# Performance work log

Measured on AMD Instinct MI355X. Metric: run time of the kernel, lower is better.

## Reference

```python
import jax, jax.numpy as jnp
import numpy as np

K = 8          # num groups
SIZE = 250     # state/hidden size (h1 = h2 = 250)
M = 576        # flattened input size (24x24)
B = 2048       # batch
HA = 100       # attention hidden
EPS = 1e-5


def _ln(x, g, b):
    mu = jnp.mean(x, axis=-1, keepdims=True)
    v = jnp.mean(jnp.square(x - mu), axis=-1, keepdims=True)
    return (x - mu) * jax.lax.rsqrt(v + EPS) * g + b


def setup_inputs() -> dict:
    key = jax.random.key(0)
    ks = jax.random.split(key, 10)
    def w(k, shape):
        return jax.random.normal(k, shape, jnp.float32) / np.sqrt(shape[0]).astype(np.float32)
    inp = {
        "x": jax.random.normal(ks[0], (B * K, M), jnp.float32),
        "state": jax.random.normal(ks[1], (B * K, SIZE), jnp.float32),
        # encoder: Linear(SIZE,250) + ReLU + LN(250)
        "enc_W": w(ks[2], (SIZE, 250)), "enc_b": jnp.zeros((250,), jnp.float32),
        "enc_g": jnp.ones((250,), jnp.float32), "enc_bt": jnp.zeros((250,), jnp.float32),
        # core: Linear(500,250) + ReLU + LN(250)
        "core_W": w(ks[3], (500, 250)), "core_b": jnp.zeros((250,), jnp.float32),
        "core_g": jnp.ones((250,), jnp.float32), "core_bt": jnp.zeros((250,), jnp.float32),
        # context: Linear(250,250) + ReLU + LN(250)
        "ctx_W": w(ks[4], (250, 250)), "ctx_b": jnp.zeros((250,), jnp.float32),
        "ctx_g": jnp.ones((250,), jnp.float32), "ctx_bt": jnp.zeros((250,), jnp.float32),
        # attention: Linear(250,100)+Tanh+LN(100)+Linear(100,1)+Sigmoid
        "att_W1": w(ks[5], (250, HA)), "att_b1": jnp.zeros((HA,), jnp.float32),
        "att_g": jnp.ones((HA,), jnp.float32), "att_bt": jnp.zeros((HA,), jnp.float32),
        "att_W2": w(ks[6], (HA, 1)), "att_b2": jnp.zeros((1,), jnp.float32),
        # output: Linear(250 + 250 + M, SIZE)
        "out_W": w(ks[7], (250 + 250 + M, SIZE)), "out_b": jnp.zeros((SIZE,), jnp.float32),
    }
    return inp


def reference(x, state, enc_W, enc_b, enc_g, enc_bt, core_W, core_b, core_g, core_bt,
              ctx_W, ctx_b, ctx_g, ctx_bt, att_W1, att_b1, att_g, att_bt,
              att_W2, att_b2, out_W, out_b):
    bk = state.shape[0]
    b = bk // K
    h1 = 250
    # 0-1. encode state -> [B*K, h1]
    s1 = _ln(jax.nn.relu(state @ enc_W + enc_b), enc_g, enc_bt)
    s1r = s1.reshape(b, K, h1)
    # 2-3. focus / context pairs via static gather index [K, K-1]
    idx = np.array([[j for j in range(K) if j != i] for i in range(K)], np.int32)
    cs = s1r[:, idx]                                    # [b, K, K-1, h1]
    fs = jnp.broadcast_to(s1r[:, :, None, :], cs.shape)  # [b, K, K-1, h1]
    # 4. concat pairs -> [b*K*(K-1), 2*h1]
    concat = jnp.concatenate([fs, cs], axis=-1).reshape(b * K * (K - 1), 2 * h1)
    # 5. core MLP
    core_out = _ln(jax.nn.relu(concat @ core_W + core_b), core_g, core_bt)
    # context MLP
    context_out = _ln(jax.nn.relu(core_out @ ctx_W + ctx_b), ctx_g, ctx_bt)
    # attention scalar per pair
    att_h = _ln(jnp.tanh(core_out @ att_W1 + att_b1), att_g, att_bt)
    att = jax.nn.sigmoid(att_h @ att_W2 + att_b2)        # [b*K*(K-1), 1]
    # 6-7. attention-weighted sum over K-1 context effects -> [B*K, h2]
    effect_sum = jnp.sum(context_out.reshape(bk, K - 1, h1) * att.reshape(bk, K - 1, 1), axis=1)
    # 8. decode
    total = jnp.concatenate([s1, effect_sum, x], axis=1)  # [B*K, h1+h2+M]
    new_state = total @ out_W + out_b                     # [B*K, SIZE]
    return new_state
```

## Files before the change

kernel.cpp:

```cpp
#include <hip/hip_runtime.h>
#include <math.h>

#define KK 8
#define H 250
#define MDIM 576
#define NB 2048
#define HA 100
#define ROWS (NB*KK)
#define PROWS (ROWS*7)
#define PQS 512
#define KP 1088
#define CSLD 352
#define EPS 1e-5f

typedef unsigned short ushort_t;
typedef short short8 __attribute__((ext_vector_type(8)));
typedef unsigned short us8 __attribute__((ext_vector_type(8)));
typedef unsigned short us4 __attribute__((ext_vector_type(4)));
typedef unsigned short us2 __attribute__((ext_vector_type(2)));
typedef float f32x4 __attribute__((ext_vector_type(4)));

__device__ __forceinline__ void wave_reduce2(float& a, float& b) {
#pragma unroll
    for (int m = 1; m < 64; m <<= 1) {
        a += __shfl_xor(a, m, 64);
        b += __shfl_xor(b, m, 64);
    }
}

__device__ __forceinline__ void async_copy16(const void* g, void* l) {
    __builtin_amdgcn_global_load_lds(
        (const __attribute__((address_space(1))) void*)g,
        (__attribute__((address_space(3))) void*)l, 16, 0, 0);
}

__device__ __forceinline__ ushort_t f2bf(float v) {
    union { float f; unsigned int u; } c; c.f = v;
    unsigned int x = c.u;
    x += 0x7fff + ((x >> 16) & 1);
    return (ushort_t)(x >> 16);
}
__device__ __forceinline__ float bf2f(ushort_t v) {
    union { unsigned int u; float f; } c; c.u = ((unsigned int)v) << 16;
    return c.f;
}
__device__ __forceinline__ float ftanh(float x) {
    const float e = __expf(2.f * x);
    return 1.f - 2.f * __builtin_amdgcn_rcpf(e + 1.f);
}
__device__ __forceinline__ float fsigmoid(float x) {
    return __builtin_amdgcn_rcpf(1.f + __expf(-x));
}

__global__ __launch_bounds__(256) void k_prep(
    const float* __restrict__ out_W, const float* __restrict__ core_W,
    const float* __restrict__ ctx_W, const float* __restrict__ att_W1,
    const float* __restrict__ enc_W, const float* __restrict__ state,
    const float* __restrict__ x,
    ushort_t* __restrict__ Wt, ushort_t* __restrict__ Wpq,
    ushort_t* __restrict__ Wca, ushort_t* __restrict__ Wenc,
    ushort_t* __restrict__ Sb, ushort_t* __restrict__ Abuf)
{
    const int b = blockIdx.x, t = threadIdx.x;
    if (b < 256) {
        const int n = b;
        for (int k = t; k < KP; k += 256) {
            const float v = (n < H && k < 1076) ? out_W[(size_t)k * H + n] : 0.f;
            Wt[(size_t)n * KP + k] = f2bf(v);
        }
    } else if (b < 768) {
        const int n = b - 256, k = t;
        float v = 0.f;
        if (k < H) {
            if (n < H)                    v = core_W[(size_t)k * H + n];
            else if (n >= 256 && n < 506) v = core_W[(size_t)(H + k) * H + (n - 256)];
        }
        Wpq[(size_t)n * 256 + k] = f2bf(v);
    } else if (b < 1152) {
        const int n = b - 768, k = t;
        float v = 0.f;
        if (k < H) {
            if (n < H)           v = ctx_W[(size_t)k * H + n];
            else if (n < H + HA) v = att_W1[(size_t)k * HA + (n - H)];
        }
        Wca[(size_t)n * 256 + k] = f2bf(v);
    } else if (b < 1408) {
        const int n = b - 1152, k = t;
        const float v = (n < H && k < H) ? enc_W[(size_t)k * H + n] : 0.f;
        Wenc[(size_t)n * 256 + k] = f2bf(v);
    } else if (b < 2432) {
        const int r0 = (b - 1408) * 16;
        for (int idx = t; idx < 16 * 256; idx += 256) {
            const int r = r0 + (idx >> 8), k = idx & 255;
            const float v = (k < H) ? state[(size_t)r * H + k] : 0.f;
            Sb[(size_t)r * 256 + k] = f2bf(v);
        }
    } else {
        const int row = b - 2432;
        for (int c = 500 + t; c < KP; c += 256) {
            const float v = (c < 500 + MDIM) ? x[(size_t)row * MDIM + (c - 500)] : 0.f;
            Abuf[(size_t)row * KP + c] = f2bf(v);
        }
    }
}

__global__ __launch_bounds__(256) void k_gemm(
    const ushort_t* __restrict__ A, int lda,
    const ushort_t* __restrict__ B, int ldb,
    void* __restrict__ Cp, int ldc,
    const float* __restrict__ bias,
    int ksteps, int ntiles, int nlim, int bf16out)
{
    __shared__ __align__(16) ushort_t As[64 * 32];
    __shared__ __align__(16) ushort_t Bs[64 * 32];
    const int tid  = threadIdx.x;
    const int lane = tid & 63, wave = tid >> 6;
    const int wm = wave >> 1, wn = wave & 1;
    const int m0 = ((int)blockIdx.x / ntiles) * 64;
    const int n0 = ((int)blockIdx.x % ntiles) * 64;

    const int srow = tid >> 2;
    const int cs   = tid & 3;
    const int cl   = cs ^ ((srow >> 1) & 3);
    const ushort_t* gA = A + (size_t)(m0 + srow) * lda + cl * 8;
    const ushort_t* gB = B + (size_t)(n0 + srow) * ldb + cl * 8;
    ushort_t* lA = &As[tid * 8];
    ushort_t* lB = &Bs[tid * 8];

    const int q  = lane >> 4;
    const int fr = lane & 15;
    int aoff[2], boff[2];
#pragma unroll
    for (int s = 0; s < 2; ++s) {
        const int ra = wm * 32 + s * 16 + fr;
        aoff[s] = (ra * 4 + (q ^ ((ra >> 1) & 3))) * 8;
        const int rb = wn * 32 + s * 16 + fr;
        boff[s] = (rb * 4 + (q ^ ((rb >> 1) & 3))) * 8;
    }

    f32x4 acc[2][2] = {};
    for (int ks = 0; ks < ksteps; ++ks) {
        const int k0 = ks * 32;
        async_copy16(gA + k0, lA);
        async_copy16(gB + k0, lB);
        __syncthreads();
        short8 a[2], b[2];
#pragma unroll
        for (int s = 0; s < 2; ++s) {
            a[s] = *(const short8*)&As[aoff[s]];
            b[s] = *(const short8*)&Bs[boff[s]];
        }
#pragma unroll
        for (int ms = 0; ms < 2; ++ms)
#pragma unroll
            for (int ns = 0; ns < 2; ++ns)
                acc[ms][ns] = __builtin_amdgcn_mfma_f32_16x16x32_bf16(
                    a[ms], b[ns], acc[ms][ns], 0, 0, 0);
        __syncthreads();
    }

#pragma unroll
    for (int ms = 0; ms < 2; ++ms)
#pragma unroll
        for (int ns = 0; ns < 2; ++ns) {
            const int n_abs = n0 + wn * 32 + ns * 16 + fr;
            if (n_abs >= nlim) continue;
            const float bv = bias ? bias[n_abs] : 0.f;
#pragma unroll
            for (int reg = 0; reg < 4; ++reg) {
                const int m_abs = m0 + wm * 32 + ms * 16 + q * 4 + reg;
                const float v = acc[ms][ns][reg] + bv;
                if (bf16out) ((ushort_t*)Cp)[(size_t)m_abs * ldc + n_abs] = f2bf(v);
                else         ((float*)Cp)[(size_t)m_abs * ldc + n_abs] = v;
            }
        }
}

__global__ __launch_bounds__(256) void k_lnenc(const ushort_t* __restrict__ Epre,
    const float* __restrict__ eb, const float* __restrict__ eg,
    const float* __restrict__ ebt, ushort_t* __restrict__ Abuf)
{
    const int wave = threadIdx.x >> 6, lane = threadIdx.x & 63;
    const int row = blockIdx.x * 4 + wave;
    const int c0 = 4 * lane;

    const us4 v = *(const us4*)&Epre[(size_t)row * 256 + c0];
    float y[4]; float sm = 0.f, sq = 0.f;
#pragma unroll
    for (int t = 0; t < 4; ++t) {
        const int cc = c0 + t;
        float z = 0.f;
        if (cc < H) z = fmaxf(bf2f(v[t]) + eb[cc], 0.f);
        y[t] = z; sm += z; sq += z * z;
    }
    wave_reduce2(sm, sq);
    const float mu = sm * (1.f / H);
    const float rs = __builtin_amdgcn_rsqf(sq * (1.f / H) - mu * mu + EPS);
    ushort_t o[4];
#pragma unroll
    for (int t = 0; t < 4; ++t) {
        const int cc = c0 + t;
        o[t] = (cc < H) ? f2bf((y[t] - mu) * rs * eg[cc] + ebt[cc]) : (ushort_t)0;
    }
    ushort_t* dst = Abuf + (size_t)row * KP + c0;
    if (c0 + 3 < H) { *(us4*)dst = (us4){o[0], o[1], o[2], o[3]}; }
    else {
        if (c0 + 1 < H) *(us2*)dst = (us2){o[0], o[1]};
    }
}

__global__ __launch_bounds__(256) void k_core(const ushort_t* __restrict__ PQb,
    const float* __restrict__ core_b, const float* __restrict__ core_g,
    const float* __restrict__ core_bt, ushort_t* __restrict__ Co)
{
    const int wave = threadIdx.x >> 6, lane = threadIdx.x & 63;
    const int g = blockIdx.x * 4 + wave;
    const int i = g & 7;
    const int c = lane * 4;

    const us4 pu = *(const us4*)&PQb[(size_t)g * PQS + c];
    us4 qu[7];
#pragma unroll
    for (int jj = 0; jj < 7; ++jj) {
        const int j = jj + (jj >= i ? 1 : 0);
        const int qr = (g & ~7) + j;
        qu[jj] = *(const us4*)&PQb[(size_t)qr * PQS + 256 + c];
    }
    float pe[4], cb[4], cg[4], cbt[4]; bool vl[4];
#pragma unroll
    for (int t = 0; t < 4; ++t) {
        vl[t]  = (c + t) < H;
        pe[t]  = bf2f(pu[t]);
        cb[t]  = vl[t] ? core_b[c + t]  : 0.f;
        cg[t]  = vl[t] ? core_g[c + t]  : 0.f;
        cbt[t] = vl[t] ? core_bt[c + t] : 0.f;
    }
    float z[7][4], red[7][2];
#pragma unroll
    for (int jj = 0; jj < 7; ++jj) {
        float sm = 0.f, sq = 0.f;
#pragma unroll
        for (int t = 0; t < 4; ++t) {
            const float zz = vl[t] ? fmaxf(pe[t] + bf2f(qu[jj][t]) + cb[t], 0.f) : 0.f;
            z[jj][t] = zz; sm += zz; sq = fmaf(zz, zz, sq);
        }
        red[jj][0] = sm; red[jj][1] = sq;
    }
#pragma unroll
    for (int m = 1; m < 64; m <<= 1)
#pragma unroll
        for (int jj = 0; jj < 7; ++jj) {
            red[jj][0] += __shfl_xor(red[jj][0], m, 64);
            red[jj][1] += __shfl_xor(red[jj][1], m, 64);
        }
#pragma unroll
    for (int jj = 0; jj < 7; ++jj) {
        const float mu = red[jj][0] * (1.f / H);
        const float rs = __builtin_amdgcn_rsqf(red[jj][1] * (1.f / H) - mu * mu + EPS);
        us4 o;
#pragma unroll
        for (int t = 0; t < 4; ++t)
            o[t] = vl[t] ? f2bf((z[jj][t] - mu) * rs * cg[t] + cbt[t]) : (ushort_t)0;
        *(us4*)&Co[((size_t)g * 7 + jj) * 256 + c] = o;
    }
}

__global__ __launch_bounds__(512, 4) void k_cs(
    const ushort_t* __restrict__ Co,
    const ushort_t* __restrict__ Wca,
    ushort_t* __restrict__ Cs)
{
    __shared__ __align__(16) ushort_t As[64 * 32];
    __shared__ __align__(16) ushort_t Bs[384 * 32];
    const int tid = threadIdx.x, lane = tid & 63, wave = tid >> 6;
    const int wm = wave >> 2, wn = wave & 3;
    const int R0 = (int)blockIdx.x * 64;

    const int ar = tid >> 2, acb = tid & 3;
    const bool aon = tid < 256;
    const int acl = acb ^ ((ar >> 1) & 3);
    const ushort_t* gA = Co + (size_t)(R0 + ar) * 256 + acl * 8;

    const int q = lane >> 4, fr = lane & 15;

    f32x4 acc[2][6] = {};
    for (int ks = 0; ks < 8; ++ks) {
        const int k0 = ks * 32;
        if (aon) async_copy16(gA + k0, &As[tid * 8]);
#pragma unroll
        for (int it = 0; it < 3; ++it) {
            const int ci  = it * 512 + tid;
            const int rb  = ci >> 2, cb2 = ci & 3;
            const int clb = cb2 ^ ((rb >> 1) & 3);
            async_copy16(Wca + (size_t)rb * 256 + k0 + clb * 8, &Bs[ci * 8]);
        }
        __syncthreads();
        short8 a[2];
#pragma unroll
        for (int ms = 0; ms < 2; ++ms) {
            const int row = wm * 32 + ms * 16 + fr;
            a[ms] = *(const short8*)&As[(row * 4 + (q ^ ((row >> 1) & 3))) * 8];
        }
#pragma unroll
        for (int nt = 0; nt < 6; ++nt) {
            const int n = wn * 96 + nt * 16 + fr;
            const short8 b = *(const short8*)&Bs[(n * 4 + (q ^ ((n >> 1) & 3))) * 8];
#pragma unroll
            for (int ms = 0; ms < 2; ++ms)
                acc[ms][nt] = __builtin_amdgcn_mfma_f32_16x16x32_bf16(
                    a[ms], b, acc[ms][nt], 0, 0, 0);
        }
        __syncthreads();
    }

#pragma unroll
    for (int ms = 0; ms < 2; ++ms)
#pragma unroll
        for (int nt = 0; nt < 6; ++nt) {
            const int col = wn * 96 + nt * 16 + fr;
            if (col >= CSLD) continue;
#pragma unroll
            for (int reg = 0; reg < 4; ++reg) {
                const int row = R0 + wm * 32 + ms * 16 + q * 4 + reg;
                Cs[(size_t)row * CSLD + col] = f2bf(acc[ms][nt][reg]);
            }
        }
}

__global__ __launch_bounds__(256) void k_eff(const ushort_t* __restrict__ Cs,
    const float* __restrict__ ctx_b, const float* __restrict__ ctx_g, const float* __restrict__ ctx_bt,
    const float* __restrict__ att_b1, const float* __restrict__ att_g, const float* __restrict__ att_bt,
    const float* __restrict__ attW2, const float* __restrict__ att_b2,
    ushort_t* __restrict__ Abuf)
{
    const int wave = threadIdx.x >> 6, lane = threadIdx.x & 63;
    const int g = blockIdx.x * 4 + wave;
    const int c0 = 4 * lane;
    const int c1 = 256 + 2 * lane;
    const bool l48 = lane < 48;

    int ce[6]; bool eC[6], eA[6]; float b_[6], g_[6], bt_[6], w2_[6], gw[6];
#pragma unroll
    for (int e = 0; e < 6; ++e) {
        ce[e] = (e < 4) ? (c0 + e) : (c1 + (e - 4));
        const bool vld = (e < 4) || l48;
        eC[e] = vld && (ce[e] < H);
        eA[e] = vld && (ce[e] >= H) && (ce[e] < H + HA);
        if (eC[e])      { b_[e] = ctx_b[ce[e]]; g_[e] = ctx_g[ce[e]]; bt_[e] = ctx_bt[ce[e]]; w2_[e] = 0.f; }
        else if (eA[e]) { const int ca = ce[e] - H;
                          b_[e] = att_b1[ca]; g_[e] = att_g[ca]; bt_[e] = att_bt[ca]; w2_[e] = attW2[ca]; }
        else            { b_[e] = g_[e] = bt_[e] = w2_[e] = 0.f; }
        gw[e] = eA[e] ? g_[e] * w2_[e] : 0.f;
    }
    float sgw = 0.f, sbw = 0.f;
#pragma unroll
    for (int e = 0; e < 6; ++e) if (eA[e]) {
        sgw += g_[e] * w2_[e];
        sbw += bt_[e] * w2_[e];
    }
    wave_reduce2(sgw, sbw);
    const float ab2 = att_b2[0] + sbw;

    us4 v0[7]; us2 v1[7];
#pragma unroll
    for (int jj = 0; jj < 7; ++jj) {
        const size_t base = ((size_t)g * 7 + jj) * CSLD;
        v0[jj] = *(const us4*)&Cs[base + c0];
        v1[jj] = l48 ? *(const us2*)&Cs[base + c1] : (us2){0, 0};
    }

    float z[7][4], red[7][5];
#pragma unroll
    for (int jj = 0; jj < 7; ++jj) {
        float smc = 0.f, sqc = 0.f, sma = 0.f, sqa = 0.f, szgw = 0.f;
#pragma unroll
        for (int e = 0; e < 6; ++e) {
            const float raw = (e < 4) ? bf2f(v0[jj][e]) : bf2f(v1[jj][e - 4]);
            float zz = 0.f;
            if (eC[e]) {
                zz = fmaxf(raw + b_[e], 0.f);
                smc += zz; sqc = fmaf(zz, zz, sqc);
            } else if (eA[e]) {
                const float za = ftanh(raw + b_[e]);
                sma += za; sqa = fmaf(za, za, sqa);
                szgw = fmaf(za, gw[e], szgw);
            }
            if (e < 4) z[jj][e] = zz;
        }
        red[jj][0] = smc; red[jj][1] = sqc; red[jj][2] = sma;
        red[jj][3] = sqa; red[jj][4] = szgw;
    }

#pragma unroll
    for (int m = 1; m < 64; m <<= 1)
#pragma unroll
        for (int jj = 0; jj < 7; ++jj)
#pragma unroll
            for (int v = 0; v < 5; ++v)
                red[jj][v] += __shfl_xor(red[jj][v], m, 64);

    float A4[4] = {0.f, 0.f, 0.f, 0.f};
    float S0 = 0.f, S1 = 0.f;
#pragma unroll
    for (int jj = 0; jj < 7; ++jj) {
        const float muC = red[jj][0] * (1.f / H);
        const float rsC = __builtin_amdgcn_rsqf(red[jj][1] * (1.f / H) - muC * muC + EPS);
        const float muA = red[jj][2] * (1.f / HA);
        const float rsA = __builtin_amdgcn_rsqf(red[jj][3] * (1.f / HA) - muA * muA + EPS);
        const float dot = rsA * (red[jj][4] - muA * sgw) + ab2;
        const float ag  = fsigmoid(dot);
        const float cj  = ag * rsC;
        S0 += ag; S1 = fmaf(cj, muC, S1);
#pragma unroll
        for (int e = 0; e < 4; ++e) A4[e] = fmaf(cj, z[jj][e], A4[e]);
    }
    ushort_t o[4];
#pragma unroll
    for (int e = 0; e < 4; ++e)
        o[e] = f2bf(g_[e] * (A4[e] - S1) + bt_[e] * S0);
    ushort_t* dst = Abuf + (size_t)g * KP + H + c0;
    if (c0 + 1 < H) *(us2*)dst       = (us2){o[0], o[1]};
    if (c0 + 3 < H) *(us2*)(dst + 2) = (us2){o[2], o[3]};
}

extern "C" void kernel_launch(void* const* d_in, const int* in_sizes, int n_in,
                              void* d_out, int out_size, void* d_ws, size_t ws_size,
                              hipStream_t stream)
{
    const float* x      = (const float*)d_in[0];
    const float* state  = (const float*)d_in[1];
    const float* enc_W  = (const float*)d_in[2];
    const float* enc_b  = (const float*)d_in[3];
    const float* enc_g  = (const float*)d_in[4];
    const float* enc_bt = (const float*)d_in[5];
    const float* core_W = (const float*)d_in[6];
    const float* core_b = (const float*)d_in[7];
    const float* core_g = (const float*)d_in[8];
    const float* core_bt= (const float*)d_in[9];
    const float* ctx_W  = (const float*)d_in[10];
    const float* ctx_b  = (const float*)d_in[11];
    const float* ctx_g  = (const float*)d_in[12];
    const float* ctx_bt = (const float*)d_in[13];
    const float* att_W1 = (const float*)d_in[14];
    const float* att_b1 = (const float*)d_in[15];
    const float* att_g  = (const float*)d_in[16];
    const float* att_bt = (const float*)d_in[17];
    const float* att_W2 = (const float*)d_in[18];
    const float* att_b2 = (const float*)d_in[19];
    const float* out_W  = (const float*)d_in[20];
    const float* out_b  = (const float*)d_in[21];
    float* out = (float*)d_out;

    ushort_t* Abuf = (ushort_t*)d_ws;
    ushort_t* Wt   = Abuf + (size_t)ROWS * KP;
    ushort_t* Wpq  = Wt + (size_t)256 * KP;
    ushort_t* Wca  = Wpq + (size_t)512 * 256;
    ushort_t* Wenc = Wca + (size_t)384 * 256;
    ushort_t* Co   = Wenc + (size_t)256 * 256;
    ushort_t* Cs   = Co + (size_t)PROWS * 256;
    ushort_t* Sb   = Cs;
    ushort_t* Epre = Sb + (size_t)ROWS * 256;
    ushort_t* PQb  = Epre + (size_t)ROWS * 256;

    k_prep  <<<2432 + ROWS, 256, 0, stream>>>(out_W, core_W, ctx_W, att_W1, enc_W,
                                              state, x, Wt, Wpq, Wca, Wenc, Sb, Abuf);
    k_gemm  <<<(ROWS / 64) * 4, 256, 0, stream>>>(Sb, 256, Wenc, 256, Epre, 256,
                                                  nullptr, 8, 4, 256, 1);
    k_lnenc <<<ROWS / 4, 256, 0, stream>>>(Epre, enc_b, enc_g, enc_bt, Abuf);
    k_gemm  <<<(ROWS / 64) * 8, 256, 0, stream>>>(Abuf, KP, Wpq, 256, PQb, PQS,
                                                  nullptr, 8, 8, 512, 1);
    k_core  <<<ROWS / 4, 256, 0, stream>>>(PQb, core_b, core_g, core_bt, Co);
    k_cs    <<<PROWS / 64, 512, 0, stream>>>(Co, Wca, Cs);
    k_eff   <<<ROWS / 4, 256, 0, stream>>>(Cs, ctx_b, ctx_g, ctx_bt,
                                           att_b1, att_g, att_bt, att_W2, att_b2,
                                           Abuf);
    k_gemm  <<<(ROWS / 64) * 4, 256, 0, stream>>>(Abuf, KP, Wt, KP, out, H,
                                                  out_b, KP / 32, 4, H, 0);
}
```

Baseline: 336.2 us.

## Use full-N-resident GEMM tiles and DPP-based wave reductions

The generic 64x64 tiled GEMM is replaced with a templated kernel where each 512-thread block owns 64 rows and the full N width (256 or 512 columns). Each A tile is loaded once per block instead of once per N tile, which removes redundant A traffic and launches fewer blocks. Separately, shuffle-xor butterfly reductions in the layernorm and attention kernels are replaced by DPP row/broadcast adds followed by a readlane. The larger B tiles raise LDS and register use per block, which may reduce occupancy.

```diff
diff --git a/kernel.cpp b/kernel.cpp
--- a/kernel.cpp
+++ b/kernel.cpp
@@ -20,12 +20,21 @@
 typedef unsigned short us2 __attribute__((ext_vector_type(2)));
 typedef float f32x4 __attribute__((ext_vector_type(4)));
 
-__device__ __forceinline__ void wave_reduce2(float& a, float& b) {
-#pragma unroll
-    for (int m = 1; m < 64; m <<= 1) {
-        a += __shfl_xor(a, m, 64);
-        b += __shfl_xor(b, m, 64);
-    }
+template<int CTRL>
+__device__ __forceinline__ float dpp_add_f32(float x) {
+    const int s = __builtin_amdgcn_update_dpp(
+        0, __builtin_bit_cast(int, x), CTRL, 0xF, 0xF, true);
+    return x + __builtin_bit_cast(float, s);
+}
+__device__ __forceinline__ float wave_sum_dpp(float x) {
+    x = dpp_add_f32<0x111>(x);
+    x = dpp_add_f32<0x112>(x);
+    x = dpp_add_f32<0x114>(x);
+    x = dpp_add_f32<0x118>(x);
+    x = dpp_add_f32<0x142>(x);
+    x = dpp_add_f32<0x143>(x);
+    return __builtin_bit_cast(float, __builtin_amdgcn_readlane(
+        __builtin_bit_cast(int, x), 63));
 }
 
 __device__ __forceinline__ void async_copy16(const void* g, void* l) {
@@ -104,74 +113,71 @@
     }
 }
 
-__global__ __launch_bounds__(256) void k_gemm(
+template<int NT>
+__global__ __launch_bounds__(512, NT == 8 ? 2 : 4) void k_gemm_nres(
     const ushort_t* __restrict__ A, int lda,
     const ushort_t* __restrict__ B, int ldb,
     void* __restrict__ Cp, int ldc,
     const float* __restrict__ bias,
-    int ksteps, int ntiles, int nlim, int bf16out)
-{
+    int ksteps, int nlim, int bf16out)
+{
+    constexpr int NROWS = NT * 64;
     __shared__ __align__(16) ushort_t As[64 * 32];
-    __shared__ __align__(16) ushort_t Bs[64 * 32];
-    const int tid  = threadIdx.x;
-    const int lane = tid & 63, wave = tid >> 6;
-    const int wm = wave >> 1, wn = wave & 1;
-    const int m0 = ((int)blockIdx.x / ntiles) * 64;
-    const int n0 = ((int)blockIdx.x % ntiles) * 64;
-
-    const int srow = tid >> 2;
-    const int cs   = tid & 3;
-    const int cl   = cs ^ ((srow >> 1) & 3);
-    const ushort_t* gA = A + (size_t)(m0 + srow) * lda + cl * 8;
-    const ushort_t* gB = B + (size_t)(n0 + srow) * ldb + cl * 8;
-    ushort_t* lA = &As[tid * 8];
-    ushort_t* lB = &Bs[tid * 8];
-
-    const int q  = lane >> 4;
-    const int fr = lane & 15;
-    int aoff[2], boff[2];
-#pragma unroll
-    for (int s = 0; s < 2; ++s) {
-        const int ra = wm * 32 + s * 16 + fr;
-        aoff[s] = (ra * 4 + (q ^ ((ra >> 1) & 3))) * 8;
-        const int rb = wn * 32 + s * 16 + fr;
-        boff[s] = (rb * 4 + (q ^ ((rb >> 1) & 3))) * 8;
-    }
-
-    f32x4 acc[2][2] = {};
+    __shared__ __align__(16) ushort_t Bs[NROWS * 32];
+    const int tid = threadIdx.x, lane = tid & 63, wave = tid >> 6;
+    const int wm = wave >> 2, wn = wave & 3;
+    const int R0 = (int)blockIdx.x * 64;
+
+    const int ar = tid >> 2, acb = tid & 3;
+    const bool aon = tid < 256;
+    const int acl = acb ^ ((ar >> 1) & 3);
+    const ushort_t* gA = A + (size_t)(R0 + ar) * lda + acl * 8;
+
+    const int q = lane >> 4, fr = lane & 15;
+
+    f32x4 acc[2][NT] = {};
     for (int ks = 0; ks < ksteps; ++ks) {
         const int k0 = ks * 32;
-        async_copy16(gA + k0, lA);
-        async_copy16(gB + k0, lB);
+        if (aon) async_copy16(gA + k0, &As[tid * 8]);
+#pragma unroll
+        for (int it = 0; it < NT / 2; ++it) {
+            const int ci  = it * 512 + tid;
+            const int rb  = ci >> 2, cb2 = ci & 3;
+            const int clb = cb2 ^ ((rb >> 1) & 3);
+            async_copy16(B + (size_t)rb * ldb + k0 + clb * 8, &Bs[ci * 8]);
+        }
         __syncthreads();
-        short8 a[2], b[2];
-#pragma unroll
-        for (int s = 0; s < 2; ++s) {
-            a[s] = *(const short8*)&As[aoff[s]];
-            b[s] = *(const short8*)&Bs[boff[s]];
-        }
-#pragma unroll
-        for (int ms = 0; ms < 2; ++ms)
-#pragma unroll
-            for (int ns = 0; ns < 2; ++ns)
-                acc[ms][ns] = __builtin_amdgcn_mfma_f32_16x16x32_bf16(
-                    a[ms], b[ns], acc[ms][ns], 0, 0, 0);
+        short8 a[2];
+#pragma unroll
+        for (int ms = 0; ms < 2; ++ms) {
+            const int row = wm * 32 + ms * 16 + fr;
+            a[ms] = *(const short8*)&As[(row * 4 + (q ^ ((row >> 1) & 3))) * 8];
+        }
+#pragma unroll
+        for (int nt = 0; nt < NT; ++nt) {
+            const int n = wn * (NT * 16) + nt * 16 + fr;
+            const short8 b = *(const short8*)&Bs[(n * 4 + (q ^ ((n >> 1) & 3))) * 8];
+#pragma unroll
+            for (int ms = 0; ms < 2; ++ms)
+                acc[ms][nt] = __builtin_amdgcn_mfma_f32_16x16x32_bf16(
+                    a[ms], b, acc[ms][nt], 0, 0, 0);
+        }
         __syncthreads();
     }
 
 #pragma unroll
     for (int ms = 0; ms < 2; ++ms)
 #pragma unroll
-        for (int ns = 0; ns < 2; ++ns) {
-            const int n_abs = n0 + wn * 32 + ns * 16 + fr;
-            if (n_abs >= nlim) continue;
-            const float bv = bias ? bias[n_abs] : 0.f;
+        for (int nt = 0; nt < NT; ++nt) {
+            const int col = wn * (NT * 16) + nt * 16 + fr;
+            if (col >= nlim) continue;
+            const float bv = bias ? bias[col] : 0.f;
 #pragma unroll
             for (int reg = 0; reg < 4; ++reg) {
-                const int m_abs = m0 + wm * 32 + ms * 16 + q * 4 + reg;
-                const float v = acc[ms][ns][reg] + bv;
-                if (bf16out) ((ushort_t*)Cp)[(size_t)m_abs * ldc + n_abs] = f2bf(v);
-                else         ((float*)Cp)[(size_t)m_abs * ldc + n_abs] = v;
+                const int row = R0 + wm * 32 + ms * 16 + q * 4 + reg;
+                const float v = acc[ms][nt][reg] + bv;
+                if (bf16out) ((ushort_t*)Cp)[(size_t)row * ldc + col] = f2bf(v);
+                else         ((float*)Cp)[(size_t)row * ldc + col] = v;
             }
         }
 }
@@ -193,7 +199,8 @@
         if (cc < H) z = fmaxf(bf2f(v[t]) + eb[cc], 0.f);
         y[t] = z; sm += z; sq += z * z;
     }
-    wave_reduce2(sm, sq);
+    sm = wave_sum_dpp(sm);
+    sq = wave_sum_dpp(sq);
     const float mu = sm * (1.f / H);
     const float rs = __builtin_amdgcn_rsqf(sq * (1.f / H) - mu * mu + EPS);
     ushort_t o[4];
@@ -247,12 +254,10 @@
         red[jj][0] = sm; red[jj][1] = sq;
     }
 #pragma unroll
-    for (int m = 1; m < 64; m <<= 1)
-#pragma unroll
-        for (int jj = 0; jj < 7; ++jj) {
-            red[jj][0] += __shfl_xor(red[jj][0], m, 64);
-            red[jj][1] += __shfl_xor(red[jj][1], m, 64);
-        }
+    for (int jj = 0; jj < 7; ++jj) {
+        red[jj][0] = wave_sum_dpp(red[jj][0]);
+        red[jj][1] = wave_sum_dpp(red[jj][1]);
+    }
 #pragma unroll
     for (int jj = 0; jj < 7; ++jj) {
         const float mu = red[jj][0] * (1.f / H);
@@ -358,7 +363,8 @@
         sgw += g_[e] * w2_[e];
         sbw += bt_[e] * w2_[e];
     }
-    wave_reduce2(sgw, sbw);
+    sgw = wave_sum_dpp(sgw);
+    sbw = wave_sum_dpp(sbw);
     const float ab2 = att_b2[0] + sbw;
 
     us4 v0[7]; us2 v1[7];
@@ -392,12 +398,10 @@
     }
 
 #pragma unroll
-    for (int m = 1; m < 64; m <<= 1)
-#pragma unroll
-        for (int jj = 0; jj < 7; ++jj)
-#pragma unroll
-            for (int v = 0; v < 5; ++v)
-                red[jj][v] += __shfl_xor(red[jj][v], m, 64);
+    for (int jj = 0; jj < 7; ++jj)
+#pragma unroll
+        for (int v = 0; v < 5; ++v)
+            red[jj][v] = wave_sum_dpp(red[jj][v]);
 
     float A4[4] = {0.f, 0.f, 0.f, 0.f};
     float S0 = 0.f, S1 = 0.f;
@@ -464,16 +468,16 @@
 
     k_prep  <<<2432 + ROWS, 256, 0, stream>>>(out_W, core_W, ctx_W, att_W1, enc_W,
                                               state, x, Wt, Wpq, Wca, Wenc, Sb, Abuf);
-    k_gemm  <<<(ROWS / 64) * 4, 256, 0, stream>>>(Sb, 256, Wenc, 256, Epre, 256,
-                                                  nullptr, 8, 4, 256, 1);
+    k_gemm_nres<4><<<ROWS / 64, 512, 0, stream>>>(Sb, 256, Wenc, 256, Epre, 256,
+                                                  nullptr, 8, 256, 1);
     k_lnenc <<<ROWS / 4, 256, 0, stream>>>(Epre, enc_b, enc_g, enc_bt, Abuf);
-    k_gemm  <<<(ROWS / 64) * 8, 256, 0, stream>>>(Abuf, KP, Wpq, 256, PQb, PQS,
-                                                  nullptr, 8, 8, 512, 1);
+    k_gemm_nres<8><<<ROWS / 64, 512, 0, stream>>>(Abuf, KP, Wpq, 256, PQb, PQS,
+                                                  nullptr, 8, 512, 1);
     k_core  <<<ROWS / 4, 256, 0, stream>>>(PQb, core_b, core_g, core_bt, Co);
     k_cs    <<<PROWS / 64, 512, 0, stream>>>(Co, Wca, Cs);
     k_eff   <<<ROWS / 4, 256, 0, stream>>>(Cs, ctx_b, ctx_g, ctx_bt,
                                            att_b1, att_g, att_bt, att_W2, att_b2,
                                            Abuf);
-    k_gemm  <<<(ROWS / 64) * 4, 256, 0, stream>>>(Abuf, KP, Wt, KP, out, H,
-                                                  out_b, KP / 32, 4, H, 0);
-}
+    k_gemm_nres<4><<<ROWS / 64, 512, 0, stream>>>(Abuf, KP, Wt, KP, out, H,
+                                                  out_b, KP / 32, 250, 0);
+}
```

Result: faster. 324.8 us (-3.4%).
